# Optimization experiments

Measured on AMD Instinct MI355X. Metric: run time of the kernel, lower is better.

The kernel has to match this reference:

```python
import jax, jax.numpy as jnp
import numpy as np

VOXEL_SIZE = 0.4
GAMMA = 1.1  # VoxelPointsSampler.GAMMA
PC_MIN, PC_MAX = -75.2, 75.2


def setup_inputs() -> dict:
    key = jax.random.key(0)
    ks = jax.random.split(key, 6)
    N, M, C, S = 200000, 256, 5, 128
    xy = jax.random.uniform(ks[0], (N, 2), minval=PC_MIN, maxval=PC_MAX)
    z = jax.random.uniform(ks[1], (N, 1), minval=-2.0, maxval=4.0)
    feat = jax.random.normal(ks[2], (N, C - 3))
    points = jnp.concatenate([xy, z, feat], axis=1)  # [N, 5]
    ctr = jax.random.uniform(ks[3], (M, 2), minval=PC_MIN * 0.9, maxval=PC_MAX * 0.9)
    cz = jnp.zeros((M, 1), jnp.float32)
    dims = jax.random.uniform(ks[4], (M, 3), minval=1.0, maxval=5.0)
    yaw = jax.random.uniform(ks[5], (M, 1), minval=-3.14, maxval=3.14)
    boxes = jnp.concatenate([ctr, cz, dims, yaw], axis=1)  # [M, 7]
    pc_start = jnp.array([PC_MIN, PC_MIN], dtype=jnp.float32)
    return {"points": points, "boxes": boxes, "pc_start": pc_start, "num_sample": S}


def reference(points, boxes, pc_start, num_sample):
    N, C = points.shape
    M = boxes.shape[0]
    # --- voxel-level radius ball query (distances in voxel units) ---
    pcoords = (points[:, :2] - pc_start) / VOXEL_SIZE          # [N, 2]
    qcoords = (boxes[:, :2] - pc_start) / VOXEL_SIZE           # [M, 2]
    r_vox = jnp.linalg.norm(boxes[:, 3:5] * 0.5, axis=-1) * GAMMA / VOXEL_SIZE  # [M]
    dist = jnp.linalg.norm(qcoords[:, None, :] - pcoords[None, :, :], axis=-1)  # [M, N]
    vmask = (dist < r_vox[:, None]).any(axis=0)                # [N]
    # --- cylindrical pool (metric space); invalid points pushed out of every radius ---
    BIG = jnp.asarray(1e6, points.dtype)
    xy_m = jnp.where(vmask[:, None], points[:, :2], BIG)       # [N, 2]
    radii = jnp.linalg.norm(boxes[:, 3:5] * 0.5, axis=-1) * GAMMA  # [M]
    dis = jnp.linalg.norm(boxes[:, None, :2] - xy_m[None, :, :], axis=-1)  # [M, N]
    pmask = (dis <= radii[:, None]).astype(points.dtype)       # 0/1 [M, N]
    sm, sidx = jax.lax.top_k(pmask, num_sample)                # [M, S]
    smb = sm > 0.5                                             # bool [M, S]
    # unique indices across all sampled slots (fixed-size for jit)
    uniq, inv = jnp.unique(sidx.ravel(), return_inverse=True,
                           size=M * num_sample, fill_value=0)
    query_points = points[uniq]                                # [M*S, C] (padded)
    sampled_points = points[sidx] * smb[:, :, None]            # [M, S, C]
    idx = inv.reshape(M, num_sample).astype(jnp.int32) * smb   # [M, S]
    return sampled_points, idx, query_points
```

## Files before the change

### kernel.cpp

```cpp
#include <hip/hip_runtime.h>

typedef unsigned long long u64;
typedef unsigned short u16;
typedef unsigned char u8;

#define VOX 0.4f
#define GAM 1.1f
#define NCX 16
#define CELLW 32.0f
#define CAP 64

__device__ __forceinline__ float dist2d(float ax, float ay, float bx, float by) {
  float dx = __fsub_rn(ax, bx);
  float dy = __fsub_rn(ay, by);
  return __fsqrt_rn(__fadd_rn(__fmul_rn(dx, dx), __fmul_rn(dy, dy)));
}

__device__ __forceinline__ float box_radius(const float* __restrict__ boxes, int m) {
  float hx = __fmul_rn(boxes[m * 7 + 3], 0.5f);
  float hy = __fmul_rn(boxes[m * 7 + 4], 0.5f);
  float nr = __fsqrt_rn(__fadd_rn(__fmul_rn(hx, hx), __fmul_rn(hy, hy)));
  return __fmul_rn(nr, GAM);
}

__device__ __forceinline__ void box_voxel(const float* __restrict__ boxes, int m,
                                          float psx, float psy,
                                          float& qx, float& qy, float& r) {
  qx = __fdiv_rn(__fsub_rn(boxes[m * 7 + 0], psx), VOX);
  qy = __fdiv_rn(__fsub_rn(boxes[m * 7 + 1], psy), VOX);
  float hx = __fmul_rn(boxes[m * 7 + 3], 0.5f);
  float hy = __fmul_rn(boxes[m * 7 + 4], 0.5f);
  float nr = __fsqrt_rn(__fadd_rn(__fmul_rn(hx, hx), __fmul_rn(hy, hy)));
  r = __fdiv_rn(__fmul_rn(nr, GAM), VOX);
}

__global__ void k_prep1(const float* __restrict__ boxes, const float* __restrict__ pc_start,
                        float* __restrict__ qxv, float* __restrict__ qyv,
                        float* __restrict__ rv, int M) {
  const int m = threadIdx.x;
  if (m < M) {
    float qx, qy, r;
    box_voxel(boxes, m, pc_start[0], pc_start[1], qx, qy, r);
    qxv[m] = qx; qyv[m] = qy; rv[m] = r;
  }
}

__global__ void k_prep2(const float* __restrict__ boxes, const float* __restrict__ pc_start,
                        int* __restrict__ cellCnt, u16* __restrict__ cellList, int M) {
  const int cell = blockIdx.x;
  const int cx = cell & (NCX - 1), cy = cell >> 4;
  const int tid = threadIdx.x;
  const int wv = tid >> 6, lane = tid & 63;
  __shared__ int wcnt[4];
  const float x0 = (cx == 0) ? -3e38f : cx * CELLW;
  const float x1 = (cx == NCX - 1) ? 3e38f : (cx + 1) * CELLW;
  const float y0 = (cy == 0) ? -3e38f : cy * CELLW;
  const float y1 = (cy == NCX - 1) ? 3e38f : (cy + 1) * CELLW;
  bool hit = false;
  if (tid < M) {
    float qx, qy, r;
    box_voxel(boxes, tid, pc_start[0], pc_start[1], qx, qy, r);
    float ddx = fmaxf(0.0f, fmaxf(x0 - qx, qx - x1));
    float ddy = fmaxf(0.0f, fmaxf(y0 - qy, qy - y1));
    float rr = r + 0.01f;
    hit = (ddx * ddx + ddy * ddy <= rr * rr);
  }
  u64 b = __ballot(hit);
  if (lane == 0) wcnt[wv] = __popcll(b);
  __syncthreads();
  int base = 0;
  for (int w = 0; w < wv; ++w) base += wcnt[w];
  if (hit) {
    int slot = base + __popcll(b & ((1ULL << lane) - 1ULL));
    if (slot < CAP) cellList[cell * CAP + slot] = (u16)tid;
  }
  if (tid == 0) cellCnt[cell] = wcnt[0] + wcnt[1] + wcnt[2] + wcnt[3];
}

__global__ void k_vmask_count(const float* __restrict__ pts, const float* __restrict__ boxes,
                              const float* __restrict__ qxv, const float* __restrict__ qyv,
                              const float* __restrict__ rv,
                              const int* __restrict__ cellCnt, const u16* __restrict__ cellList,
                              u64* __restrict__ vbits, u8* __restrict__ present,
                              int* __restrict__ cnt,
                              float* __restrict__ cpxg, float* __restrict__ cpyg,
                              int* __restrict__ cpng, int* __restrict__ nflags,
                              const float* __restrict__ pc_start,
                              int N, int M, int nchunk) {
  __shared__ float cpx[256], cpy[256];
  __shared__ int cpn[256];
  __shared__ int wcnt[4];
  const int tid = threadIdx.x;
  const int blk = blockIdx.x;
  const int n = blk * 256 + tid;
  const int wv = tid >> 6, lane = tid & 63;
  const float psx = pc_start[0], psy = pc_start[1];
  const bool valid = (n < N);
  float px = 1e6f, py = 1e6f, pvx = 0.f, pvy = 0.f;
  if (valid) {
    px = pts[n * 5 + 0];
    py = pts[n * 5 + 1];
    pvx = __fdiv_rn(__fsub_rn(px, psx), VOX);
    pvy = __fdiv_rn(__fsub_rn(py, psy), VOX);
    present[n] = 0;
  }

  bool flag = false;
  if (valid) {
    int cx = (int)floorf(pvx * (1.0f / CELLW));
    int cy = (int)floorf(pvy * (1.0f / CELLW));
    cx = cx < 0 ? 0 : (cx > NCX - 1 ? NCX - 1 : cx);
    cy = cy < 0 ? 0 : (cy > NCX - 1 ? NCX - 1 : cy);
    const int cell = cy * NCX + cx;
    const int k = cellCnt[cell];
    if (k <= CAP) {
      for (int j = 0; j < k; ++j) {
        const int m = cellList[cell * CAP + j];
        float d = dist2d(qxv[m], qyv[m], pvx, pvy);
        if (d < rv[m]) { flag = true; break; }
      }
    } else {
      for (int m = 0; m < M; ++m) {
        float d = dist2d(qxv[m], qyv[m], pvx, pvy);
        if (d < rv[m]) { flag = true; break; }
      }
    }
  }
  u64 b = __ballot(flag);
  if (lane == 0) {
    vbits[n >> 6] = b;
    wcnt[wv] = __popcll(b);
  }
  __syncthreads();

  int base = 0;
  for (int w = 0; w < wv; ++w) base += wcnt[w];
  if (flag) {
    int slot = base + __popcll(b & ((1ULL << lane) - 1ULL));
    cpx[slot] = px;
    cpy[slot] = py;
    cpn[slot] = n;
  }
  __syncthreads();
  const int nfl = wcnt[0] + wcnt[1] + wcnt[2] + wcnt[3];
  if (tid == 0) nflags[blk] = nfl;
  if (tid < nfl) {
    cpxg[blk * 256 + tid] = cpx[tid];
    cpyg[blk * 256 + tid] = cpy[tid];
    cpng[blk * 256 + tid] = cpn[tid];
  }

  for (int t0 = 0; t0 < M; t0 += 256) {
    const int bm = t0 + tid;
    if (bm < M) {
      const float bx = boxes[bm * 7 + 0], by = boxes[bm * 7 + 1];
      const float r = box_radius(boxes, bm);
      int c = 0;
      for (int j = 0; j < nfl; ++j) {
        float d = dist2d(bx, by, cpx[j], cpy[j]);
        c += (d <= r) ? 1 : 0;
      }
      cnt[bm * nchunk + blk] = c;
    }
  }
}

__global__ void __launch_bounds__(1024) k_scanbox(const int* __restrict__ cnt,
                                                  int* __restrict__ off,
                                                  int* __restrict__ kcount,
                                                  int nchunk, int M, int S) {
  __shared__ int s[1024];
  const int m = blockIdx.x, t = threadIdx.x;
  int v = (t < nchunk) ? cnt[m * nchunk + t] : 0;
  s[t] = v;
  __syncthreads();
  for (int d = 1; d < 1024; d <<= 1) {
    int x = (t >= d) ? s[t - d] : 0;
    __syncthreads();
    s[t] += x;
    __syncthreads();
  }
  if (t < nchunk) off[t * M + m] = s[t] - v;
  if (t == 1023) kcount[m] = (s[t] < S) ? s[t] : S;
}

__global__ void k_fillz(const float* __restrict__ pts, const float* __restrict__ boxes,
                        const float* __restrict__ cpxg, const float* __restrict__ cpyg,
                        const int* __restrict__ cpng, const int* __restrict__ nflags,
                        const int* __restrict__ off, const u64* __restrict__ vbits,
                        const int* __restrict__ kcount,
                        int* __restrict__ sidx, u8* __restrict__ present,
                        int N, int M, int S, int nchunk) {
  __shared__ float sx[256], sy[256];
  __shared__ int sn[256];
  if ((int)blockIdx.x < nchunk) {
    const int c = blockIdx.x;
    const int tid = threadIdx.x;
    const int nf = nflags[c];
    if (nf == 0) return;
    if (tid < nf) {
      sx[tid] = cpxg[c * 256 + tid];
      sy[tid] = cpyg[c * 256 + tid];
      sn[tid] = cpng[c * 256 + tid];
    }
    __syncthreads();
    for (int m = tid; m < M; m += 256) {
      int cum = off[c * M + m];
      if (cum >= S) continue;
      const float bx = boxes[m * 7 + 0], by = boxes[m * 7 + 1];
      const float r = box_radius(boxes, m);
      for (int j = 0; j < nf; ++j) {
        float d = dist2d(bx, by, sx[j], sy[j]);
        if (d <= r) {
          int pn = sn[j];
          sidx[m * S + cum] = pn;
          present[pn] = 1;
          if (++cum >= S) break;
        }
      }
    }
  } else {
    const int m = blockIdx.x - nchunk;
    const int k0 = kcount[m];
    if (k0 >= S) return;
    const int lane = threadIdx.x;
    if (lane >= 64) return;
    const float bx = boxes[m * 7 + 0], by = boxes[m * 7 + 1];
    const float r = box_radius(boxes, m);
    const u64 ltmask = (1ULL << lane) - 1ULL;
    const int nwords = (N + 63) >> 6;
    int fill = k0;
    for (int wi = 0; wi < nwords && fill < S; ++wi) {
      const u64 w = vbits[wi];
      const int n = (wi << 6) + lane;
      bool one = false;
      if (n < N && ((w >> lane) & 1ULL)) {
        float d = dist2d(bx, by, pts[n * 5 + 0], pts[n * 5 + 1]);
        one = (d <= r);
      }
      const bool z = (n < N) && !one;
      u64 b = __ballot(z);
      if (z) {
        int pos = fill + __popcll(b & ltmask);
        if (pos < S) { sidx[m * S + pos] = n; present[n] = 1; }
      }
      fill += __popcll(b);
    }
  }
}

__global__ void k_bsum(const u8* __restrict__ present, int* __restrict__ bsum, int N) {
  const int n = blockIdx.x * 256 + threadIdx.x;
  bool f = (n < N) && present[n];
  u64 b = __ballot(f);
  __shared__ int ws[4];
  if ((threadIdx.x & 63) == 0) ws[threadIdx.x >> 6] = __popcll(b);
  __syncthreads();
  if (threadIdx.x == 0) bsum[blockIdx.x] = ws[0] + ws[1] + ws[2] + ws[3];
}

__global__ void __launch_bounds__(1024) k_scan(const int* __restrict__ bsum,
                                               int* __restrict__ boff, int nb) {
  __shared__ int s[1024];
  const int t = threadIdx.x;
  int v = (t < nb) ? bsum[t] : 0;
  s[t] = v;
  __syncthreads();
  for (int d = 1; d < 1024; d <<= 1) {
    int x = (t >= d) ? s[t - d] : 0;
    __syncthreads();
    s[t] += x;
    __syncthreads();
  }
  boff[t] = s[t] - v;
  if (t == nb - 1) boff[1024] = s[t];
}

__global__ void k_rank(const u8* __restrict__ present, const int* __restrict__ boff,
                       const float* __restrict__ pts, int* __restrict__ rank_arr,
                       float* __restrict__ out_query, int N) {
  const int t = threadIdx.x;
  const int n = blockIdx.x * 256 + t;
  bool f = (n < N) && present[n];
  u64 b = __ballot(f);
  __shared__ int ws[4];
  const int wv = t >> 6, lane = t & 63;
  if (lane == 0) ws[wv] = __popcll(b);
  __syncthreads();
  int base = boff[blockIdx.x];
  for (int w = 0; w < wv; ++w) base += ws[w];
  if (f) {
    int rank = base + __popcll(b & ((1ULL << lane) - 1ULL));
    rank_arr[n] = rank;
    float* q = out_query + (size_t)rank * 5;
    const float* p = pts + (size_t)n * 5;
    q[0] = p[0]; q[1] = p[1]; q[2] = p[2]; q[3] = p[3]; q[4] = p[4];
  }
}

__global__ void k_outpad(const float* __restrict__ pts, const int* __restrict__ sidx,
                         const int* __restrict__ kcount, const int* __restrict__ rank_arr,
                         const int* __restrict__ uptr,
                         float* __restrict__ out_samp, float* __restrict__ out_idx,
                         float* __restrict__ out_query, int MS, int S) {
  const int e = blockIdx.x * 256 + threadIdx.x;
  if (e >= MS) return;
  const int U = *uptr;
  if (e >= U) {
    float* q = out_query + (size_t)e * 5;
    q[0] = pts[0]; q[1] = pts[1]; q[2] = pts[2]; q[3] = pts[3]; q[4] = pts[4];
  }
  const int m = e / S;
  const int s = e - m * S;
  float* o = out_samp + (size_t)e * 5;
  if (s < kcount[m]) {
    int n = sidx[e];
    const float* p = pts + (size_t)n * 5;
    o[0] = p[0]; o[1] = p[1]; o[2] = p[2]; o[3] = p[3]; o[4] = p[4];
    out_idx[e] = (float)rank_arr[n];
  } else {
    o[0] = 0.f; o[1] = 0.f; o[2] = 0.f; o[3] = 0.f; o[4] = 0.f;
    out_idx[e] = 0.f;
  }
}

extern "C" void kernel_launch(void* const* d_in, const int* in_sizes, int n_in,
                              void* d_out, int out_size, void* d_ws, size_t ws_size,
                              hipStream_t stream) {
  const float* pts = (const float*)d_in[0];
  const float* boxes = (const float*)d_in[1];
  const float* pc_start = (const float*)d_in[2];
  const int N = in_sizes[0] / 5;
  const int M = in_sizes[1] / 7;
  const int S = out_size / (M * 11);
  const int MS = M * S;

  float* out_samp = (float*)d_out;
  float* out_idx = out_samp + (size_t)MS * 5;
  float* out_query = out_idx + (size_t)MS;

  const int nb = (N + 255) / 256;
  const int nchunk = nb;

  char* w = (char*)d_ws;
  auto take = [&](size_t bytes) {
    char* p = w;
    w += (bytes + 15) & ~(size_t)15;
    return (void*)p;
  };
  u64* vbits     = (u64*)take((size_t)(nb * 4) * 8);
  int* cnt       = (int*)take((size_t)M * nchunk * 4);
  int* off       = (int*)take((size_t)nchunk * M * 4);
  float* cpxg    = (float*)take((size_t)nchunk * 256 * 4);
  float* cpyg    = (float*)take((size_t)nchunk * 256 * 4);
  int* cpng      = (int*)take((size_t)nchunk * 256 * 4);
  int* nflags    = (int*)take((size_t)nchunk * 4);
  int* sidx      = (int*)take((size_t)MS * 4);
  int* kcount    = (int*)take((size_t)M * 4);
  int* rank_arr  = (int*)take((size_t)N * 4);
  int* bsum      = (int*)take((size_t)1024 * 4);
  int* boff      = (int*)take((size_t)1025 * 4);
  u8*  present   = (u8*)take((size_t)N);
  float* qxv     = (float*)take((size_t)M * 4);
  float* qyv     = (float*)take((size_t)M * 4);
  float* rv      = (float*)take((size_t)M * 4);
  int* cellCnt   = (int*)take((size_t)NCX * NCX * 4);
  u16* cellList  = (u16*)take((size_t)NCX * NCX * CAP * 2);

  k_prep1<<<1, 256, 0, stream>>>(boxes, pc_start, qxv, qyv, rv, M);
  k_prep2<<<NCX * NCX, 256, 0, stream>>>(boxes, pc_start, cellCnt, cellList, M);
  k_vmask_count<<<nb, 256, 0, stream>>>(pts, boxes, qxv, qyv, rv, cellCnt, cellList,
                                        vbits, present, cnt, cpxg, cpyg, cpng, nflags,
                                        pc_start, N, M, nchunk);
  k_scanbox<<<M, 1024, 0, stream>>>(cnt, off, kcount, nchunk, M, S);
  k_fillz<<<nchunk + M, 256, 0, stream>>>(pts, boxes, cpxg, cpyg, cpng, nflags, off,
                                          vbits, kcount, sidx, present, N, M, S, nchunk);
  k_bsum<<<nb, 256, 0, stream>>>(present, bsum, N);
  k_scan<<<1, 1024, 0, stream>>>(bsum, boff, nb);
  k_rank<<<nb, 256, 0, stream>>>(present, boff, pts, rank_arr, out_query, N);
  k_outpad<<<(MS + 255) / 256, 256, 0, stream>>>(pts, sidx, kcount, rank_arr, boff + 1024,
                                                 out_samp, out_idx, out_query, MS, S);
}
```

Baseline: 103.8 us.

## Compute per-chunk box membership bitmasks via cell lists, reuse in fill

Instead of every box testing every flagged point in a chunk (M×nfl distance tests, done twice), each flagged point tests only the boxes listed for its spatial cell and sets a bit in a per-box shared bitmask with atomicOr. Counts come from popcount, and the bitmasks are written to global memory so the fill kernel walks set bits rather than recomputing distances. The two prep kernels are merged into one launch. In exchange there is a larger workspace (chunks×M×32 bytes), traffic for the bitmask writes and reads, and shared-memory atomics. The fill stage now handles one box per thread and covers at most 256 boxes, which fits M=256 here.

```diff
diff --git a/kernel.cpp b/kernel.cpp
--- a/kernel.cpp
+++ b/kernel.cpp
@@ -34,22 +34,20 @@
   r = __fdiv_rn(__fmul_rn(nr, GAM), VOX);
 }
 
-__global__ void k_prep1(const float* __restrict__ boxes, const float* __restrict__ pc_start,
-                        float* __restrict__ qxv, float* __restrict__ qyv,
-                        float* __restrict__ rv, int M) {
-  const int m = threadIdx.x;
-  if (m < M) {
-    float qx, qy, r;
-    box_voxel(boxes, m, pc_start[0], pc_start[1], qx, qy, r);
-    qxv[m] = qx; qyv[m] = qy; rv[m] = r;
-  }
-}
-
-__global__ void k_prep2(const float* __restrict__ boxes, const float* __restrict__ pc_start,
-                        int* __restrict__ cellCnt, u16* __restrict__ cellList, int M) {
-  const int cell = blockIdx.x;
+__global__ void k_prep(const float* __restrict__ boxes, const float* __restrict__ pc_start,
+                       float* __restrict__ qxv, float* __restrict__ qyv, float* __restrict__ rv,
+                       int* __restrict__ cellCnt, u16* __restrict__ cellList, int M) {
+  const int tid = threadIdx.x;
+  if (blockIdx.x == 0) {
+    for (int m = tid; m < M; m += 256) {
+      float qx, qy, r;
+      box_voxel(boxes, m, pc_start[0], pc_start[1], qx, qy, r);
+      qxv[m] = qx; qyv[m] = qy; rv[m] = r;
+    }
+    return;
+  }
+  const int cell = blockIdx.x - 1;
   const int cx = cell & (NCX - 1), cy = cell >> 4;
-  const int tid = threadIdx.x;
   const int wv = tid >> 6, lane = tid & 63;
   __shared__ int wcnt[4];
   const float x0 = (cx == 0) ? -3e38f : cx * CELLW;
@@ -82,13 +80,14 @@
                               const float* __restrict__ rv,
                               const int* __restrict__ cellCnt, const u16* __restrict__ cellList,
                               u64* __restrict__ vbits, u8* __restrict__ present,
-                              int* __restrict__ cnt,
-                              float* __restrict__ cpxg, float* __restrict__ cpyg,
-                              int* __restrict__ cpng, int* __restrict__ nflags,
+                              int* __restrict__ cnt, u64* __restrict__ bmG,
+                              int* __restrict__ cpng,
                               const float* __restrict__ pc_start,
                               int N, int M, int nchunk) {
   __shared__ float cpx[256], cpy[256];
   __shared__ int cpn[256];
+  __shared__ float sbx[256], sby[256], sbr[256];
+  __shared__ u64 bm[256][4];
   __shared__ int wcnt[4];
   const int tid = threadIdx.x;
   const int blk = blockIdx.x;
@@ -96,6 +95,14 @@
   const int wv = tid >> 6, lane = tid & 63;
   const float psx = pc_start[0], psy = pc_start[1];
   const bool valid = (n < N);
+
+  bm[tid][0] = 0; bm[tid][1] = 0; bm[tid][2] = 0; bm[tid][3] = 0;
+  if (tid < M) {
+    sbx[tid] = boxes[tid * 7 + 0];
+    sby[tid] = boxes[tid * 7 + 1];
+    sbr[tid] = box_radius(boxes, tid);
+  }
+
   float px = 1e6f, py = 1e6f, pvx = 0.f, pvy = 0.f;
   if (valid) {
     px = pts[n * 5 + 0];
@@ -143,25 +150,41 @@
   }
   __syncthreads();
   const int nfl = wcnt[0] + wcnt[1] + wcnt[2] + wcnt[3];
-  if (tid == 0) nflags[blk] = nfl;
+  if (tid < nfl) cpng[blk * 256 + tid] = cpn[tid];
+
   if (tid < nfl) {
-    cpxg[blk * 256 + tid] = cpx[tid];
-    cpyg[blk * 256 + tid] = cpy[tid];
-    cpng[blk * 256 + tid] = cpn[tid];
-  }
-
-  for (int t0 = 0; t0 < M; t0 += 256) {
-    const int bm = t0 + tid;
-    if (bm < M) {
-      const float bx = boxes[bm * 7 + 0], by = boxes[bm * 7 + 1];
-      const float r = box_radius(boxes, bm);
-      int c = 0;
-      for (int j = 0; j < nfl; ++j) {
-        float d = dist2d(bx, by, cpx[j], cpy[j]);
-        c += (d <= r) ? 1 : 0;
-      }
-      cnt[bm * nchunk + blk] = c;
-    }
+    const float mx = cpx[tid], my = cpy[tid];
+    float vx = __fdiv_rn(__fsub_rn(mx, psx), VOX);
+    float vy = __fdiv_rn(__fsub_rn(my, psy), VOX);
+    int cx = (int)floorf(vx * (1.0f / CELLW));
+    int cy = (int)floorf(vy * (1.0f / CELLW));
+    cx = cx < 0 ? 0 : (cx > NCX - 1 ? NCX - 1 : cx);
+    cy = cy < 0 ? 0 : (cy > NCX - 1 ? NCX - 1 : cy);
+    const int cell = cy * NCX + cx;
+    const int k = cellCnt[cell];
+    const u64 bit = 1ULL << (tid & 63);
+    const int word = tid >> 6;
+    if (k <= CAP) {
+      for (int j = 0; j < k; ++j) {
+        const int m = cellList[cell * CAP + j];
+        float d = dist2d(sbx[m], sby[m], mx, my);
+        if (d <= sbr[m]) atomicOr(&bm[m][word], bit);
+      }
+    } else {
+      for (int m = 0; m < M; ++m) {
+        float d = dist2d(sbx[m], sby[m], mx, my);
+        if (d <= sbr[m]) atomicOr(&bm[m][word], bit);
+      }
+    }
+  }
+  __syncthreads();
+
+  if (tid < M) {
+    u64 w0 = bm[tid][0], w1 = bm[tid][1], w2 = bm[tid][2], w3 = bm[tid][3];
+    u64* dst = bmG + ((size_t)blk * M + tid) * 4;
+    dst[0] = w0; dst[1] = w1; dst[2] = w2; dst[3] = w3;
+    cnt[tid * nchunk + blk] =
+        __popcll(w0) + __popcll(w1) + __popcll(w2) + __popcll(w3);
   }
 }
 
@@ -185,38 +208,31 @@
 }
 
 __global__ void k_fillz(const float* __restrict__ pts, const float* __restrict__ boxes,
-                        const float* __restrict__ cpxg, const float* __restrict__ cpyg,
-                        const int* __restrict__ cpng, const int* __restrict__ nflags,
+                        const u64* __restrict__ bmG, const int* __restrict__ cpng,
                         const int* __restrict__ off, const u64* __restrict__ vbits,
                         const int* __restrict__ kcount,
                         int* __restrict__ sidx, u8* __restrict__ present,
                         int N, int M, int S, int nchunk) {
-  __shared__ float sx[256], sy[256];
-  __shared__ int sn[256];
   if ((int)blockIdx.x < nchunk) {
     const int c = blockIdx.x;
-    const int tid = threadIdx.x;
-    const int nf = nflags[c];
-    if (nf == 0) return;
-    if (tid < nf) {
-      sx[tid] = cpxg[c * 256 + tid];
-      sy[tid] = cpyg[c * 256 + tid];
-      sn[tid] = cpng[c * 256 + tid];
-    }
-    __syncthreads();
-    for (int m = tid; m < M; m += 256) {
-      int cum = off[c * M + m];
-      if (cum >= S) continue;
-      const float bx = boxes[m * 7 + 0], by = boxes[m * 7 + 1];
-      const float r = box_radius(boxes, m);
-      for (int j = 0; j < nf; ++j) {
-        float d = dist2d(bx, by, sx[j], sy[j]);
-        if (d <= r) {
-          int pn = sn[j];
-          sidx[m * S + cum] = pn;
-          present[pn] = 1;
-          if (++cum >= S) break;
-        }
+    const int m = threadIdx.x;
+    if (m >= M) return;
+    const u64* bp = bmG + ((size_t)c * M + m) * 4;
+    u64 w0 = bp[0], w1 = bp[1], w2 = bp[2], w3 = bp[3];
+    if (!(w0 | w1 | w2 | w3)) return;
+    int cum = off[c * M + m];
+    if (cum >= S) return;
+    const int* pbase = cpng + c * 256;
+    u64 ws[4] = {w0, w1, w2, w3};
+    for (int wi = 0; wi < 4 && cum < S; ++wi) {
+      u64 w = ws[wi];
+      while (w && cum < S) {
+        int j = (wi << 6) + __builtin_ctzll(w);
+        w &= w - 1;
+        int pn = pbase[j];
+        sidx[m * S + cum] = pn;
+        present[pn] = 1;
+        ++cum;
       }
     }
   } else {
@@ -351,10 +367,8 @@
   u64* vbits     = (u64*)take((size_t)(nb * 4) * 8);
   int* cnt       = (int*)take((size_t)M * nchunk * 4);
   int* off       = (int*)take((size_t)nchunk * M * 4);
-  float* cpxg    = (float*)take((size_t)nchunk * 256 * 4);
-  float* cpyg    = (float*)take((size_t)nchunk * 256 * 4);
+  u64* bmG       = (u64*)take((size_t)nchunk * M * 4 * 8);
   int* cpng      = (int*)take((size_t)nchunk * 256 * 4);
-  int* nflags    = (int*)take((size_t)nchunk * 4);
   int* sidx      = (int*)take((size_t)MS * 4);
   int* kcount    = (int*)take((size_t)M * 4);
   int* rank_arr  = (int*)take((size_t)N * 4);
@@ -367,13 +381,13 @@
   int* cellCnt   = (int*)take((size_t)NCX * NCX * 4);
   u16* cellList  = (u16*)take((size_t)NCX * NCX * CAP * 2);
 
-  k_prep1<<<1, 256, 0, stream>>>(boxes, pc_start, qxv, qyv, rv, M);
-  k_prep2<<<NCX * NCX, 256, 0, stream>>>(boxes, pc_start, cellCnt, cellList, M);
+  k_prep<<<NCX * NCX + 1, 256, 0, stream>>>(boxes, pc_start, qxv, qyv, rv,
+                                            cellCnt, cellList, M);
   k_vmask_count<<<nb, 256, 0, stream>>>(pts, boxes, qxv, qyv, rv, cellCnt, cellList,
-                                        vbits, present, cnt, cpxg, cpyg, cpng, nflags,
+                                        vbits, present, cnt, bmG, cpng,
                                         pc_start, N, M, nchunk);
   k_scanbox<<<M, 1024, 0, stream>>>(cnt, off, kcount, nchunk, M, S);
-  k_fillz<<<nchunk + M, 256, 0, stream>>>(pts, boxes, cpxg, cpyg, cpng, nflags, off,
+  k_fillz<<<nchunk + M, 256, 0, stream>>>(pts, boxes, bmG, cpng, off,
                                           vbits, kcount, sidx, present, N, M, S, nchunk);
   k_bsum<<<nb, 256, 0, stream>>>(present, bsum, N);
   k_scan<<<1, 1024, 0, stream>>>(bsum, boff, nb);
```

New measurement: 95.56 us. 7.9% less time.
